# Kernel optimization log

Hardware: AMD Instinct MI355X
Metric: run time of the kernel (lower is better)

## Reference

```python
import jax, jax.numpy as jnp
import numpy as np

EMB = 128  # embedding_size hard-coded in source
NW = 8192  # weak samples
NS = 8192  # strong samples
FD = 1024  # encoder input feature dim
QN = 1024  # queue max_size
C = 80     # num classes (COCO-style WSOD)


def setup_inputs() -> dict:
    key = jax.random.key(0)
    ks = jax.random.split(key, 9)
    return {
        "feats_strong": jax.random.normal(ks[0], (NS, FD), jnp.float32),
        "feats_weak": jax.random.normal(ks[1], (NW, FD), jnp.float32),
        "strong_labels": jax.random.randint(ks[2], (NS,), 0, C, jnp.int64),
        "weak_labels": jax.random.randint(ks[3], (NW,), 0, C, jnp.int64),
        "Wq": jax.random.normal(ks[4], (FD, EMB), jnp.float32) * (FD ** -0.5),
        "bq": jax.random.normal(ks[5], (EMB,), jnp.float32) * 0.01,
        "Wk": jax.random.normal(ks[6], (FD, EMB), jnp.float32) * (FD ** -0.5),
        "bk": jax.random.normal(ks[7], (EMB,), jnp.float32) * 0.01,
        "queue": jax.random.normal(ks[8], (QN, EMB), jnp.float32),
    }


def reference(feats_strong, feats_weak, strong_labels, weak_labels, Wq, bq, Wk, bk, queue):
    # Encoders applied to all samples at once (original loops one-by-one).
    q_all = feats_weak @ Wq + bq            # [NW, EMB]
    k_all = feats_strong @ Wk + bk          # [NS, EMB]
    k_all = jax.lax.stop_gradient(k_all)    # k = k.detach() in source

    w, s = weak_labels, strong_labels
    eq_ws = w[:, None] == s[None, :]                      # [NW, NS] weak-vs-strong label match
    cnt = eq_ws.astype(jnp.int32).sum(1)                  # num_strong per weak sample
    valid = cnt > 0                                       # `if weak_label in strong_labels`

    # rank of i among weak indices with the same label (position in torch.where output)
    eq_ww = (w[:, None] == w[None, :]).astype(jnp.int32)
    rank = jnp.tril(eq_ww, -1).sum(1)                     # [NW]
    sel = rank % jnp.maximum(cnt, 1)                      # `% num_strong`

    # occurrence rank of each strong index within its label group
    eq_ss = (s[:, None] == s[None, :]).astype(jnp.int32)
    occ = jnp.tril(eq_ss, -1).sum(1)                      # [NS]

    # index_strong[i] = sel[i]-th strong index whose label == w[i]
    M = eq_ws & (occ[None, :] == sel[:, None])            # [NW, NS]
    idx = jnp.argmax(M, axis=1)                           # [NW]

    q = q_all                                             # [NW, EMB]
    k = k_all[idx]                                        # [NW, EMB]

    l_pos = jnp.sum(q * k, axis=-1, keepdims=True)        # bmm([N,1,E],[N,E,1]) -> [N,1]
    l_neg = q @ queue.reshape(EMB, -1)                    # queue.view(EMB, -1): row-major reshape
    logits = jnp.concatenate([l_pos, l_neg], axis=1)      # [NW, 1+QN]

    # CrossEntropy with target 0 on each valid row, mean over valid rows
    ce = -jax.nn.log_softmax(logits, axis=-1)[:, 0]
    m = valid.astype(logits.dtype)
    loss = jnp.sum(ce * m) / jnp.maximum(m.sum(), 1.0)
    return loss
```

## Files before the change

kernel.cpp:

```cpp
#include <hip/hip_runtime.h>
#include <hip/hip_bf16.h>

#define NW   8192
#define NS   8192
#define FD   1024
#define EMB  128
#define QN   1024
#define NC   80

typedef unsigned short ushort_t;
typedef unsigned int   uint_t;
typedef __attribute__((ext_vector_type(8))) short short8;
typedef __attribute__((ext_vector_type(4))) float f32x4;

#define OFF_Q      0u
#define OFF_K      1048576u
#define OFF_WTQ    2097152u
#define OFF_WTK    2129920u
#define OFF_HIST   2752512u
#define OFF_RANK   2752640u
#define OFF_CNT    2760832u
#define OFF_BHS    2785408u
#define OFF_BHW    2787968u
#define OFF_ACC    2790528u
#define OFF_QT     2790532u
#define OFF_TABLE  3000000u

__device__ __forceinline__ ushort_t f2bf(float f) {
    uint_t u = __float_as_uint(f);
    u = (u + 0x7fffu + ((u >> 16) & 1u)) >> 16;
    return (ushort_t)u;
}
__device__ __forceinline__ uint_t pack2(float a, float b) {
    return (uint_t)f2bf(a) | ((uint_t)f2bf(b) << 16);
}

#define GLOAD_LDS16(gp, lp)                                                     \
    __builtin_amdgcn_global_load_lds(                                           \
        (const __attribute__((address_space(1))) void*)(gp),                    \
        (__attribute__((address_space(3))) void*)(lp), 16, 0, 0)

__global__ __launch_bounds__(256) void cvtbh_k(const float* __restrict__ Wq,
                                               const float* __restrict__ Wk,
                                               const float* __restrict__ queue,
                                               const int* __restrict__ s_lab,
                                               const int* __restrict__ w_lab,
                                               ushort_t* __restrict__ Wtq,
                                               ushort_t* __restrict__ Wtk,
                                               ushort_t* __restrict__ Qt,
                                               int* __restrict__ bhs,
                                               int* __restrict__ bhw,
                                               float* __restrict__ accum,
                                               int* __restrict__ counter) {
    int bx = blockIdx.x;
    int t = threadIdx.x;
    if (bx >= 384) {
        __shared__ int h[NC];
        int b2 = bx - 384, z = b2 >> 5, cb = b2 & 31;
        const int* lab = z ? w_lab : s_lab;
        int* bh = z ? bhw : bhs;
        if (t < NC) h[t] = 0;
        __syncthreads();
        atomicAdd(&h[lab[cb * 256 + t]], 1);
        __syncthreads();
        if (t < NC) bh[cb * NC + t] = h[t];
        return;
    }
    __shared__ float tile[32][33];
    int z = bx >> 7, flat = bx & 127;
    if (z == 0 && flat == 0) {
        if (t < 2) accum[t] = 0.0f;
        if (t == 2) *counter = 0;
    }
    const float* in; ushort_t* out; int r0, c0, C;
    if (z < 2) { in = z ? Wk : Wq; out = z ? Wtk : Wtq; C = 128;
                 r0 = (flat >> 2) * 32; c0 = (flat & 3) * 32; }
    else       { in = queue; out = Qt; C = 1024;
                 r0 = (flat & 3) * 32; c0 = (flat >> 2) * 32; }
    int i = t >> 3, j0 = (t & 7) * 4;
    float4 v = *(const float4*)(in + (size_t)(r0 + i) * C + c0 + j0);
    tile[i][j0] = v.x; tile[i][j0 + 1] = v.y; tile[i][j0 + 2] = v.z; tile[i][j0 + 3] = v.w;
    __syncthreads();
    uint2 pk;
    pk.x = pack2(tile[j0][i], tile[j0 + 1][i]);
    pk.y = pack2(tile[j0 + 2][i], tile[j0 + 3][i]);
    size_t oaddr;
    int k0 = r0 + j0, n = c0 + i;
    if (z < 2) {
        oaddr = (size_t)(k0 >> 6) * 8192 + (size_t)((k0 >> 3) & 7) * 1024
              + (size_t)n * 8 + (k0 & 7);
    } else {
        int c = k0 >> 3;
        oaddr = ((size_t)n * 16 + (c ^ (n & 15))) * 8 + (k0 & 7);
    }
    *(uint2*)(out + oaddr) = pk;
}

__global__ __launch_bounds__(256) void enc_mfma_k(const float* __restrict__ A0,
                                                  const float* __restrict__ A1,
                                                  const ushort_t* __restrict__ Wt0,
                                                  const ushort_t* __restrict__ Wt1,
                                                  const float* __restrict__ b0_,
                                                  const float* __restrict__ b1_,
                                                  float* __restrict__ out0,
                                                  float* __restrict__ out1,
                                                  const int* __restrict__ s_lab,
                                                  const int* __restrict__ w_lab,
                                                  const int* __restrict__ bhs,
                                                  const int* __restrict__ bhw,
                                                  int* __restrict__ table,
                                                  int* __restrict__ rank,
                                                  int* __restrict__ hist) {
    __shared__ __align__(16) char smem[49152];

    int bx = blockIdx.x;
    int t = threadIdx.x;

    if (bx >= 512) {
        int* ll = (int*)smem;
        int b2 = bx - 512, z = b2 >> 5, cb = b2 & 31;
        const int* lab = z ? w_lab : s_lab;
        const int* bh = z ? bhw : bhs;
        int j = cb * 256 + t;
        int c = lab[j];
        ll[t] = c;
        __syncthreads();
        int r = 0;
        for (int b = 0; b < cb; b++) r += bh[b * NC + c];
        for (int jj = 0; jj < t; jj++) r += (ll[jj] == c) ? 1 : 0;
        if (z) rank[j] = r;
        else   table[c * 8192 + r] = j;
        if (b2 == 0 && t < 128) {
            int h = 0;
            if (t < NC)
                for (int b = 0; b < 32; b++) h += bhs[b * NC + t];
            hist[t] = h;
        }
        return;
    }

    int which = bx >> 8;
    int mtile = bx & 255;
    const float*    A    = which ? A1 : A0;
    const ushort_t* Wt   = which ? Wt1 : Wt0;
    const float*    bias = which ? b1_ : b0_;
    float*          out  = which ? out1 : out0;
    int row0 = mtile * 32;

    int wv = t >> 6, ln = t & 63;
    int wm = wv >> 1, wn = wv & 1;
    int lane15 = ln & 15, kg = ln >> 4;

    int ar0 = wv * 8 + (ln >> 4);
    int ar1 = ar0 + 4;
    const float* gA0 = A + (size_t)(row0 + ar0) * FD + (((ln & 15) ^ (ar0 & 15))) * 4;
    const float* gA1 = A + (size_t)(row0 + ar1) * FD + (((ln & 15) ^ (ar1 & 15))) * 4;
    const ushort_t* gB = Wt + (size_t)wv * 2048 + ln * 8;

    f32x4 acc[4];
#pragma unroll
    for (int nt = 0; nt < 4; nt++) acc[nt] = (f32x4){0.f, 0.f, 0.f, 0.f};

#define STAGE(BUF, KB)                                                           \
    { char* lb = smem + (BUF) * 24576;                                           \
      GLOAD_LDS16(gA0 + (size_t)(KB) * 64, lb + wv * 2048);                      \
      GLOAD_LDS16(gA1 + (size_t)(KB) * 64, lb + wv * 2048 + 1024);               \
      const ushort_t* gb = gB + (size_t)(KB) * 8192;                             \
      char* bb = lb + 8192 + wv * 4096;                                          \
      GLOAD_LDS16(gb,        bb);                                                \
      GLOAD_LDS16(gb + 512,  bb + 1024);                                         \
      GLOAD_LDS16(gb + 1024, bb + 2048);                                         \
      GLOAD_LDS16(gb + 1536, bb + 3072); }

    STAGE(0, 0)
    __syncthreads();

#pragma unroll 1
    for (int kb = 0; kb < 16; kb++) {
        int cur = kb & 1;
        if (kb < 15) STAGE(cur ^ 1, kb + 1)
        char* lb = smem + cur * 24576;
#pragma unroll
        for (int ks = 0; ks < 2; ks++) {
            int r_l = wm * 16 + lane15;
            int c0 = ks * 8 + kg * 2;
            float4 alo = *(const float4*)(lb + ((size_t)r_l * 16 + ((c0)     ^ (r_l & 15))) * 16);
            float4 ahi = *(const float4*)(lb + ((size_t)r_l * 16 + ((c0 + 1) ^ (r_l & 15))) * 16);
            uint4 pk;
            pk.x = pack2(alo.x, alo.y); pk.y = pack2(alo.z, alo.w);
            pk.z = pack2(ahi.x, ahi.y); pk.w = pack2(ahi.z, ahi.w);
            short8 af = __builtin_bit_cast(short8, pk);
            int kgg = ks * 4 + kg;
#pragma unroll
            for (int nt = 0; nt < 4; nt++) {
                uint4 bb = *(const uint4*)(lb + 8192 +
                            ((size_t)kgg * 128 + wn * 64 + nt * 16 + lane15) * 16);
                acc[nt] = __builtin_amdgcn_mfma_f32_16x16x32_bf16(
                    af, __builtin_bit_cast(short8, bb), acc[nt], 0, 0, 0);
            }
        }
        __syncthreads();
    }
#undef STAGE

#pragma unroll
    for (int nt = 0; nt < 4; nt++) {
        int col = wn * 64 + nt * 16 + lane15;
        float bv = bias[col];
        int rbase = row0 + wm * 16 + kg * 4;
#pragma unroll
        for (int j = 0; j < 4; j++)
            out[(size_t)(rbase + j) * EMB + col] = acc[nt][j] + bv;
    }
}

__global__ __launch_bounds__(256, 2) void ce_mfma_k(const float* __restrict__ q,
                                                    const float* __restrict__ k,
                                                    const ushort_t* __restrict__ Qt,
                                                    const int* __restrict__ rank,
                                                    const int* __restrict__ table,
                                                    const int* __restrict__ w,
                                                    const int* __restrict__ hist,
                                                    float* __restrict__ accum,
                                                    int* __restrict__ counter,
                                                    float* __restrict__ outp) {
    __shared__ __align__(16) char bsm[32768];
    __shared__ int   idx_lds[16];
    __shared__ float lpos_lds[16];
    __shared__ float mg[4][16][2];
    int t = threadIdx.x;
    int r0 = blockIdx.x * 16;

    if (t < 16) {
        int i = r0 + t;
        int c = w[i];
        int cc = hist[c];
        idx_lds[t] = (cc > 0) ? table[c * 8192 + (rank[i] % cc)] : 0;
    }
    __syncthreads();

    {
        int rr = t >> 4;
        int o = (t & 15) * 8;
        const float4* qa = (const float4*)(q + (size_t)(r0 + rr) * EMB + o);
        const float4* ka = (const float4*)(k + (size_t)idx_lds[rr] * EMB + o);
        float4 a0 = qa[0], b0 = ka[0], a1 = qa[1], b1 = ka[1];
        float s = a0.x * b0.x + a0.y * b0.y + a0.z * b0.z + a0.w * b0.w
                + a1.x * b1.x + a1.y * b1.y + a1.z * b1.z + a1.w * b1.w;
        s += __shfl_xor(s, 1); s += __shfl_xor(s, 2);
        s += __shfl_xor(s, 4); s += __shfl_xor(s, 8);
        if ((t & 15) == 0) lpos_lds[rr] = s;
    }

    int wv = t >> 6, ln = t & 63;
    int lane15 = ln & 15, kg = ln >> 4;

    short8 afr[4];
#pragma unroll
    for (int ks = 0; ks < 4; ks++) {
        const float4* p = (const float4*)(q + (size_t)(r0 + lane15) * EMB + ks * 32 + kg * 8);
        float4 a = p[0], b = p[1];
        uint4 pk;
        pk.x = pack2(a.x, a.y); pk.y = pack2(a.z, a.w);
        pk.z = pack2(b.x, b.y); pk.w = pack2(b.z, b.w);
        afr[ks] = __builtin_bit_cast(short8, pk);
    }

    f32x4 acc[16];
#pragma unroll
    for (int nc = 0; nc < 16; nc++) acc[nc] = (f32x4){0.f, 0.f, 0.f, 0.f};

#define STAGE_CE(BUF, NC)                                                        \
    { char* lb = bsm + (BUF) * 16384;                                            \
      const ushort_t* src = Qt + (size_t)(NC) * 8192 + wv * 2048 + ln * 8;       \
      char* bb = lb + wv * 4096;                                                 \
      GLOAD_LDS16(src,        bb);                                               \
      GLOAD_LDS16(src + 512,  bb + 1024);                                        \
      GLOAD_LDS16(src + 1024, bb + 2048);                                        \
      GLOAD_LDS16(src + 1536, bb + 3072); }

    STAGE_CE(0, 0)
    __syncthreads();

#pragma unroll
    for (int nc = 0; nc < 16; nc++) {
        int cur = nc & 1;
        if (nc < 15) STAGE_CE(cur ^ 1, nc + 1)
        char* lb = bsm + cur * 16384;
        int n_l = wv * 16 + lane15;
#pragma unroll
        for (int ks = 0; ks < 4; ks++) {
            int c = ks * 4 + kg;
            uint4 bb = *(const uint4*)(lb + ((size_t)n_l * 16 + (c ^ lane15)) * 16);
            acc[nc] = __builtin_amdgcn_mfma_f32_16x16x32_bf16(
                afr[ks], __builtin_bit_cast(short8, bb), acc[nc], 0, 0, 0);
        }
        __syncthreads();
    }
#undef STAGE_CE

#pragma unroll
    for (int j = 0; j < 4; j++) {
        float mx = -1e30f;
#pragma unroll
        for (int nc = 0; nc < 16; nc++) mx = fmaxf(mx, acc[nc][j]);
        mx = fmaxf(mx, __shfl_xor(mx, 1));
        mx = fmaxf(mx, __shfl_xor(mx, 2));
        mx = fmaxf(mx, __shfl_xor(mx, 4));
        mx = fmaxf(mx, __shfl_xor(mx, 8));
        float s = 0.f;
#pragma unroll
        for (int nc = 0; nc < 16; nc++) s += __expf(acc[nc][j] - mx);
        s += __shfl_xor(s, 1);
        s += __shfl_xor(s, 2);
        s += __shfl_xor(s, 4);
        s += __shfl_xor(s, 8);
        if (lane15 == 0) {
            mg[wv][kg * 4 + j][0] = mx;
            mg[wv][kg * 4 + j][1] = s;
        }
    }
    __syncthreads();
    if (wv == 0) {
        float cv = 0.f, cc = 0.f;
        if (t < 16) {
            int i = r0 + t;
            float m0 = mg[0][t][0], l0 = mg[0][t][1];
            float m1 = mg[1][t][0], l1 = mg[1][t][1];
            float m2 = mg[2][t][0], l2 = mg[2][t][1];
            float m3 = mg[3][t][0], l3 = mg[3][t][1];
            float lp = lpos_lds[t];
            float m = fmaxf(fmaxf(fmaxf(m0, m1), fmaxf(m2, m3)), lp);
            float l = l0 * __expf(m0 - m) + l1 * __expf(m1 - m)
                    + l2 * __expf(m2 - m) + l3 * __expf(m3 - m) + __expf(lp - m);
            float ce = -(lp - m - __logf(l));
            if (hist[w[i]] > 0) { cv = ce; cc = 1.f; }
        }
        cv += __shfl_xor(cv, 1);  cc += __shfl_xor(cc, 1);
        cv += __shfl_xor(cv, 2);  cc += __shfl_xor(cc, 2);
        cv += __shfl_xor(cv, 4);  cc += __shfl_xor(cc, 4);
        cv += __shfl_xor(cv, 8);  cc += __shfl_xor(cc, 8);
        if (t == 0) {
            atomicAdd(&accum[0], cv);
            atomicAdd(&accum[1], cc);
            __threadfence();
            int done = atomicAdd(counter, 1);
            if (done == 511) {
                float s = atomicAdd(&accum[0], 0.0f);
                float c = atomicAdd(&accum[1], 0.0f);
                outp[0] = s / fmaxf(c, 1.0f);
            }
        }
    }
}

extern "C" void kernel_launch(void* const* d_in, const int* in_sizes, int n_in,
                              void* d_out, int out_size, void* d_ws, size_t ws_size,
                              hipStream_t stream) {
    const float* feats_strong = (const float*)d_in[0];
    const float* feats_weak   = (const float*)d_in[1];
    const int*   s_lab        = (const int*)d_in[2];
    const int*   w_lab        = (const int*)d_in[3];
    const float* Wq           = (const float*)d_in[4];
    const float* bq           = (const float*)d_in[5];
    const float* Wk           = (const float*)d_in[6];
    const float* bk           = (const float*)d_in[7];
    const float* queue        = (const float*)d_in[8];

    float*    wsf = (float*)d_ws;
    int*      wsi = (int*)d_ws;

    float*    q_g   = wsf + OFF_Q;
    float*    k_g   = wsf + OFF_K;
    int*      table = wsi + OFF_TABLE;
    ushort_t* Wtq   = (ushort_t*)(wsi + OFF_WTQ);
    ushort_t* Wtk   = (ushort_t*)(wsi + OFF_WTK);
    int*      hist  = wsi + OFF_HIST;
    int*      rank  = wsi + OFF_RANK;
    int*      cnt   = wsi + OFF_CNT;
    int*      bhs   = wsi + OFF_BHS;
    int*      bhw   = wsi + OFF_BHW;
    float*    accum = wsf + OFF_ACC;
    ushort_t* Qt    = (ushort_t*)(wsi + OFF_QT);

    cvtbh_k<<<448, 256, 0, stream>>>(Wq, Wk, queue, s_lab, w_lab,
                                     Wtq, Wtk, Qt, bhs, bhw, accum, cnt);
    enc_mfma_k<<<576, 256, 0, stream>>>(feats_weak, feats_strong, Wtq, Wtk, bq, bk, q_g, k_g,
                                        s_lab, w_lab, bhs, bhw, table, rank, hist);
    ce_mfma_k<<<512, 256, 0, stream>>>(q_g, k_g, Qt, rank, table, w_lab, hist,
                                       accum, cnt, (float*)d_out);
}
```

Measured before the change: 153.2 us.

## Triple-buffer LDS pipelines in encoder and CE kernels with single barrier per step

Both the encoder GEMM and the CE logits kernel move from double-buffered LDS staging to triple-buffered staging with a prefetch distance of two. Each step now uses an explicit vmcnt wait and one s_barrier instead of two __syncthreads. The label-ranking blocks are moved to the first block indices so they are scheduled before the GEMM tiles. The cost is more LDS per block (72KB and 48KB), which can lower occupancy, and hand-tuned vmcnt counts that must match the number of in-flight loads exactly.

```diff
diff --git a/kernel.cpp b/kernel.cpp
--- a/kernel.cpp
+++ b/kernel.cpp
@@ -111,14 +111,14 @@
                                                   int* __restrict__ table,
                                                   int* __restrict__ rank,
                                                   int* __restrict__ hist) {
-    __shared__ __align__(16) char smem[49152];
+    __shared__ __align__(16) char smem[73728];
 
     int bx = blockIdx.x;
     int t = threadIdx.x;
 
-    if (bx >= 512) {
+    if (bx < 64) {
         int* ll = (int*)smem;
-        int b2 = bx - 512, z = b2 >> 5, cb = b2 & 31;
+        int b2 = bx, z = b2 >> 5, cb = b2 & 31;
         const int* lab = z ? w_lab : s_lab;
         const int* bh = z ? bhw : bhs;
         int j = cb * 256 + t;
@@ -139,8 +139,9 @@
         return;
     }
 
-    int which = bx >> 8;
-    int mtile = bx & 255;
+    int bxg = bx - 64;
+    int which = bxg >> 8;
+    int mtile = bxg & 255;
     const float*    A    = which ? A1 : A0;
     const ushort_t* Wt   = which ? Wt1 : Wt0;
     const float*    bias = which ? b1_ : b0_;
@@ -162,45 +163,53 @@
     for (int nt = 0; nt < 4; nt++) acc[nt] = (f32x4){0.f, 0.f, 0.f, 0.f};
 
 #define STAGE(BUF, KB)                                                           \
-    { char* lb = smem + (BUF) * 24576;                                           \
-      GLOAD_LDS16(gA0 + (size_t)(KB) * 64, lb + wv * 2048);                      \
-      GLOAD_LDS16(gA1 + (size_t)(KB) * 64, lb + wv * 2048 + 1024);               \
+    { char* sb = smem + (BUF) * 24576;                                           \
+      GLOAD_LDS16(gA0 + (size_t)(KB) * 64, sb + wv * 2048);                      \
+      GLOAD_LDS16(gA1 + (size_t)(KB) * 64, sb + wv * 2048 + 1024);               \
       const ushort_t* gb = gB + (size_t)(KB) * 8192;                             \
-      char* bb = lb + 8192 + wv * 4096;                                          \
+      char* bb = sb + 8192 + wv * 4096;                                          \
       GLOAD_LDS16(gb,        bb);                                                \
       GLOAD_LDS16(gb + 512,  bb + 1024);                                         \
       GLOAD_LDS16(gb + 1024, bb + 2048);                                         \
       GLOAD_LDS16(gb + 1536, bb + 3072); }
 
+#define K2_ITER(KB, CURB, STB, VMSTR)                                            \
+    { asm volatile("s_waitcnt vmcnt(" VMSTR ")" ::: "memory");                   \
+      __builtin_amdgcn_s_barrier();                                              \
+      __builtin_amdgcn_sched_barrier(0);                                         \
+      if ((KB) < 14) STAGE(STB, (KB) + 2)                                        \
+      { char* lb = smem + (CURB) * 24576;                                        \
+        _Pragma("unroll")                                                        \
+        for (int ks = 0; ks < 2; ks++) {                                         \
+            int r_l = wm * 16 + lane15;                                          \
+            int c0 = ks * 8 + kg * 2;                                            \
+            float4 alo = *(const float4*)(lb + ((size_t)r_l * 16 + ((c0)     ^ (r_l & 15))) * 16); \
+            float4 ahi = *(const float4*)(lb + ((size_t)r_l * 16 + ((c0 + 1) ^ (r_l & 15))) * 16); \
+            uint4 pk;                                                            \
+            pk.x = pack2(alo.x, alo.y); pk.y = pack2(alo.z, alo.w);              \
+            pk.z = pack2(ahi.x, ahi.y); pk.w = pack2(ahi.z, ahi.w);              \
+            short8 af = __builtin_bit_cast(short8, pk);                          \
+            int kgg = ks * 4 + kg;                                               \
+            _Pragma("unroll")                                                    \
+            for (int nt = 0; nt < 4; nt++) {                                     \
+                uint4 bv = *(const uint4*)(lb + 8192 +                           \
+                            ((size_t)kgg * 128 + wn * 64 + nt * 16 + lane15) * 16); \
+                acc[nt] = __builtin_amdgcn_mfma_f32_16x16x32_bf16(               \
+                    af, __builtin_bit_cast(short8, bv), acc[nt], 0, 0, 0);       \
+            }                                                                    \
+        } }                                                                      \
+    }
+
     STAGE(0, 0)
-    __syncthreads();
-
+    STAGE(1, 1)
 #pragma unroll 1
-    for (int kb = 0; kb < 16; kb++) {
-        int cur = kb & 1;
-        if (kb < 15) STAGE(cur ^ 1, kb + 1)
-        char* lb = smem + cur * 24576;
-#pragma unroll
-        for (int ks = 0; ks < 2; ks++) {
-            int r_l = wm * 16 + lane15;
-            int c0 = ks * 8 + kg * 2;
-            float4 alo = *(const float4*)(lb + ((size_t)r_l * 16 + ((c0)     ^ (r_l & 15))) * 16);
-            float4 ahi = *(const float4*)(lb + ((size_t)r_l * 16 + ((c0 + 1) ^ (r_l & 15))) * 16);
-            uint4 pk;
-            pk.x = pack2(alo.x, alo.y); pk.y = pack2(alo.z, alo.w);
-            pk.z = pack2(ahi.x, ahi.y); pk.w = pack2(ahi.z, ahi.w);
-            short8 af = __builtin_bit_cast(short8, pk);
-            int kgg = ks * 4 + kg;
-#pragma unroll
-            for (int nt = 0; nt < 4; nt++) {
-                uint4 bb = *(const uint4*)(lb + 8192 +
-                            ((size_t)kgg * 128 + wn * 64 + nt * 16 + lane15) * 16);
-                acc[nt] = __builtin_amdgcn_mfma_f32_16x16x32_bf16(
-                    af, __builtin_bit_cast(short8, bb), acc[nt], 0, 0, 0);
-            }
-        }
-        __syncthreads();
-    }
+    for (int kb3 = 0; kb3 < 15; kb3 += 3) {
+        K2_ITER(kb3 + 0, 0, 2, "6")
+        K2_ITER(kb3 + 1, 1, 0, "6")
+        K2_ITER(kb3 + 2, 2, 1, "6")
+    }
+    K2_ITER(15, 0, 0, "0")
+#undef K2_ITER
 #undef STAGE
 
 #pragma unroll
@@ -224,7 +233,7 @@
                                                     float* __restrict__ accum,
                                                     int* __restrict__ counter,
                                                     float* __restrict__ outp) {
-    __shared__ __align__(16) char bsm[32768];
+    __shared__ __align__(16) char bsm[49152];
     __shared__ int   idx_lds[16];
     __shared__ float lpos_lds[16];
     __shared__ float mg[4][16][2];
@@ -270,23 +279,26 @@
 #pragma unroll
     for (int nc = 0; nc < 16; nc++) acc[nc] = (f32x4){0.f, 0.f, 0.f, 0.f};
 
-#define STAGE_CE(BUF, NC)                                                        \
-    { char* lb = bsm + (BUF) * 16384;                                            \
-      const ushort_t* src = Qt + (size_t)(NC) * 8192 + wv * 2048 + ln * 8;       \
-      char* bb = lb + wv * 4096;                                                 \
+#define STAGE_CE(BUF, NCK)                                                       \
+    { char* sb = bsm + (BUF) * 16384;                                            \
+      const ushort_t* src = Qt + (size_t)(NCK) * 8192 + wv * 2048 + ln * 8;      \
+      char* bb = sb + wv * 4096;                                                 \
       GLOAD_LDS16(src,        bb);                                               \
       GLOAD_LDS16(src + 512,  bb + 1024);                                        \
       GLOAD_LDS16(src + 1024, bb + 2048);                                        \
       GLOAD_LDS16(src + 1536, bb + 3072); }
 
     STAGE_CE(0, 0)
-    __syncthreads();
+    STAGE_CE(1, 1)
 
 #pragma unroll
     for (int nc = 0; nc < 16; nc++) {
-        int cur = nc & 1;
-        if (nc < 15) STAGE_CE(cur ^ 1, nc + 1)
-        char* lb = bsm + cur * 16384;
+        if (nc < 15) { asm volatile("s_waitcnt vmcnt(4)" ::: "memory"); }
+        else         { asm volatile("s_waitcnt vmcnt(0)" ::: "memory"); }
+        __builtin_amdgcn_s_barrier();
+        __builtin_amdgcn_sched_barrier(0);
+        if (nc < 14) STAGE_CE((nc + 2) % 3, nc + 2)
+        char* lb = bsm + (nc % 3) * 16384;
         int n_l = wv * 16 + lane15;
 #pragma unroll
         for (int ks = 0; ks < 4; ks++) {
@@ -295,7 +307,6 @@
             acc[nc] = __builtin_amdgcn_mfma_f32_16x16x32_bf16(
                 afr[ks], __builtin_bit_cast(short8, bb), acc[nc], 0, 0, 0);
         }
-        __syncthreads();
     }
 #undef STAGE_CE
 
```

Result: no change. 153.2 us (+0.0%).
